# Optimization experiments

Hardware: AMD Instinct MI355X
Metric: run time of the kernel (lower is better)

Reference implementation:

```python
import jax, jax.numpy as jnp
import numpy as np

NBITS = 4
GROUP_SIZE = 128


def setup_inputs() -> dict:
    key = jax.random.key(0)
    k1, k2, k3, k4, k5 = jax.random.split(key, 5)
    B, S, K, N = 2, 2048, 4096, 4096
    G = K // GROUP_SIZE  # 32 groups along K
    x = jax.random.normal(k1, (B, S, K), dtype=jnp.float16)
    # unpacked uint4 weights stored in int32 carrier, values in [0, 2^nbits)
    W_q = jax.random.randint(k2, (N, K), 0, 2 ** NBITS, dtype=jnp.int32)
    scale = (jax.random.uniform(k3, (N, G), dtype=jnp.float32) * 0.01 + 0.001).astype(jnp.float16)
    zero = (jax.random.uniform(k4, (N, G), dtype=jnp.float32) * (2 ** NBITS)).astype(jnp.float16)
    bias = jax.random.normal(k5, (N,), dtype=jnp.float16)
    return {"x": x, "W_q": W_q, "scale": scale, "zero": zero, "bias": bias}


def _dequant(W_q, scale, zero):
    # W_q: [N, K] int, scale/zero: [N, K//group_size] fp16
    # zeros_mode='original': W = (W_q - zero) * scale, per group along K
    N, K = W_q.shape
    G = K // GROUP_SIZE
    Wg = W_q.reshape(N, G, GROUP_SIZE).astype(jnp.float16)
    Wd = (Wg - zero[:, :, None]) * scale[:, :, None]
    return Wd.reshape(N, K)


def reference(x, W_q, scale, zero, bias):
    # out = x @ W_deq^T + bias   (layout 'nt': W is [N, K])
    W = _dequant(W_q, scale, zero)            # [N, K] fp16
    out = jnp.einsum('bsk,nk->bsn', x, W)     # [B, S, N] fp16 accum per module config
    return out + bias
```

## Files before the change

### kernel.cpp

```cpp
#include <hip/hip_runtime.h>
#include <hip/hip_bf16.h>


typedef __bf16 bf16x8 __attribute__((ext_vector_type(8)));
typedef float f32x4 __attribute__((ext_vector_type(4)));

#define BM 128
#define BN 128
#define BK 64

static __device__ __forceinline__ int pack_bf16x2(float a, float b) {
    __hip_bfloat162 p = __float22bfloat162_rn(make_float2(a, b));
    int r;
    __builtin_memcpy(&r, &p, 4);
    return r;
}

__global__ __launch_bounds__(256) void prepass_kernel(
    const float* __restrict__ X,
    const int*   __restrict__ Wq,
    const float* __restrict__ scale,
    const float* __restrict__ zero,
    unsigned short* __restrict__ Ad,
    unsigned short* __restrict__ Wd,
    int K, int G, int GROUP, int nWBlocks)
{
    const int b = blockIdx.x;
    if (b < nWBlocks) {
        const unsigned int idx = (unsigned int)b * 256u + threadIdx.x;
        const unsigned int f = idx * 8u;
        const unsigned int n = f / (unsigned int)K;
        const unsigned int k = f - n * (unsigned int)K;
        const unsigned int g = k / (unsigned int)GROUP;
        const float s  = scale[(size_t)n * G + g];
        const float z  = zero [(size_t)n * G + g];
        const float mz = -z * s;
        const int4 q0 = *(const int4*)(Wq + f);
        const int4 q1 = *(const int4*)(Wq + f + 4);
        int4 d;
        d.x = pack_bf16x2((float)q0.x * s + mz, (float)q0.y * s + mz);
        d.y = pack_bf16x2((float)q0.z * s + mz, (float)q0.w * s + mz);
        d.z = pack_bf16x2((float)q1.x * s + mz, (float)q1.y * s + mz);
        d.w = pack_bf16x2((float)q1.z * s + mz, (float)q1.w * s + mz);
        *(int4*)(Wd + f) = d;
    } else {
        const unsigned int idx = (unsigned int)(b - nWBlocks) * 256u + threadIdx.x;
        const unsigned int f = idx * 8u;
        const float4 a0 = *(const float4*)(X + f);
        const float4 a1 = *(const float4*)(X + f + 4);
        int4 d;
        d.x = pack_bf16x2(a0.x, a0.y);
        d.y = pack_bf16x2(a0.z, a0.w);
        d.z = pack_bf16x2(a1.x, a1.y);
        d.w = pack_bf16x2(a1.z, a1.w);
        *(int4*)(Ad + f) = d;
    }
}

__global__ __launch_bounds__(256, 2) void gemm_bf16_nt(
    const unsigned short* __restrict__ A,
    const unsigned short* __restrict__ Bw,
    const float* __restrict__ bias,
    float*       __restrict__ C,
    int M, int N, int K)
{
    __shared__ unsigned short ldsA[BM * BK];
    __shared__ unsigned short ldsB[BN * BK];

    const int tid   = threadIdx.x;
    const int lane  = tid & 63;
    const int wave  = tid >> 6;
    const int waveM = wave >> 1;
    const int waveN = wave & 1;

    const int blockN0 = blockIdx.x * BN;
    const int blockM0 = blockIdx.y * BM;

    const long long aBase = (long long)blockM0 * K;
    const long long bBase = (long long)blockN0 * K;

    const int rowInChunk = lane >> 3;
    const int col8       = ((lane & 7) ^ rowInChunk) * 8;

    f32x4 acc[4][4];
#pragma unroll
    for (int i = 0; i < 4; ++i)
#pragma unroll
        for (int j = 0; j < 4; ++j)
            acc[i][j] = (f32x4){0.f, 0.f, 0.f, 0.f};

    const int row16 = lane & 15;
    const int quad  = lane >> 4;
    const int sw    = row16 & 7;

    for (int k0 = 0; k0 < K; k0 += BK) {
        __syncthreads();
#pragma unroll
        for (int c = 0; c < 4; ++c) {
            const int chunk = (wave << 2) | c;
            const int row   = (chunk << 3) | rowInChunk;
            const unsigned short* gA = A  + aBase + (long long)row * K + k0 + col8;
            const unsigned short* gB = Bw + bBase + (long long)row * K + k0 + col8;
            __builtin_amdgcn_global_load_lds(
                (const __attribute__((address_space(1))) unsigned int*)gA,
                (__attribute__((address_space(3))) unsigned int*)&ldsA[chunk * 512],
                16, 0, 0);
            __builtin_amdgcn_global_load_lds(
                (const __attribute__((address_space(1))) unsigned int*)gB,
                (__attribute__((address_space(3))) unsigned int*)&ldsB[chunk * 512],
                16, 0, 0);
        }
        __syncthreads();

#pragma unroll
        for (int kk = 0; kk < 2; ++kk) {
            bf16x8 av[4], bv[4];
            const int slot = (kk * 4 + quad) ^ sw;
#pragma unroll
            for (int i = 0; i < 4; ++i) {
                const int r = waveM * 64 + i * 16 + row16;
                av[i] = *(const bf16x8*)&ldsA[r * BK + slot * 8];
            }
#pragma unroll
            for (int j = 0; j < 4; ++j) {
                const int r = waveN * 64 + j * 16 + row16;
                bv[j] = *(const bf16x8*)&ldsB[r * BK + slot * 8];
            }
#pragma unroll
            for (int i = 0; i < 4; ++i)
#pragma unroll
                for (int j = 0; j < 4; ++j)
                    acc[i][j] = __builtin_amdgcn_mfma_f32_16x16x32_bf16(
                        av[i], bv[j], acc[i][j], 0, 0, 0);
        }
    }

    const int colBase = blockN0 + waveN * 64;
    const int rowBase = blockM0 + waveM * 64;
    float biasf[4];
#pragma unroll
    for (int j = 0; j < 4; ++j)
        biasf[j] = bias[colBase + j * 16 + row16];

#pragma unroll
    for (int i = 0; i < 4; ++i) {
        const int row0 = rowBase + i * 16 + quad * 4;
#pragma unroll
        for (int j = 0; j < 4; ++j) {
            const int col = colBase + j * 16 + row16;
#pragma unroll
            for (int r = 0; r < 4; ++r) {
                C[(long long)(row0 + r) * N + col] = acc[i][j][r] + biasf[j];
            }
        }
    }
}

__global__ __launch_bounds__(256) void hqq_gemm_fused_f32(
    const float* __restrict__ A,
    const int*   __restrict__ Wq,
    const float* __restrict__ scale,
    const float* __restrict__ zero,
    const float* __restrict__ bias,
    float*       __restrict__ C,
    int M, int N, int K, int G, int GROUP)
{
    __shared__ unsigned short ldsA[BM * BK];
    __shared__ unsigned short ldsB[BN * BK];

    const int tid   = threadIdx.x;
    const int lane  = tid & 63;
    const int wave  = tid >> 6;
    const int waveM = wave >> 1;
    const int waveN = wave & 1;

    const int blockN0 = blockIdx.x * BN;
    const int blockM0 = blockIdx.y * BM;

    const int row16 = lane & 15;
    const int quad  = lane >> 4;

    f32x4 acc[4][4];
#pragma unroll
    for (int i = 0; i < 4; ++i)
#pragma unroll
        for (int j = 0; j < 4; ++j)
            acc[i][j] = (f32x4){0.f, 0.f, 0.f, 0.f};

    for (int k0 = 0; k0 < K; k0 += BK) {
        const int g = k0 / GROUP;
        int4 ra[4], rb[4];
#pragma unroll
        for (int c = 0; c < 4; ++c) {
            const int chunk = c * 256 + tid;
            const int row   = chunk >> 3;
            const int col   = (chunk & 7) * 8;

            const float* ap = A + (long long)(blockM0 + row) * K + k0 + col;
            const float4 a0 = *(const float4*)(ap);
            const float4 a1 = *(const float4*)(ap + 4);
            int4 da;
            da.x = pack_bf16x2(a0.x, a0.y);
            da.y = pack_bf16x2(a0.z, a0.w);
            da.z = pack_bf16x2(a1.x, a1.y);
            da.w = pack_bf16x2(a1.z, a1.w);
            ra[c] = da;

            const int n = blockN0 + row;
            const float s  = scale[(long long)n * G + g];
            const float z  = zero [(long long)n * G + g];
            const float mz = -z * s;
            const long long wb = (long long)n * K + k0 + col;
            const int4 q0 = *(const int4*)(Wq + wb);
            const int4 q1 = *(const int4*)(Wq + wb + 4);
            int4 db;
            db.x = pack_bf16x2((float)q0.x * s + mz, (float)q0.y * s + mz);
            db.y = pack_bf16x2((float)q0.z * s + mz, (float)q0.w * s + mz);
            db.z = pack_bf16x2((float)q1.x * s + mz, (float)q1.y * s + mz);
            db.w = pack_bf16x2((float)q1.z * s + mz, (float)q1.w * s + mz);
            rb[c] = db;
        }

        __syncthreads();
#pragma unroll
        for (int c = 0; c < 4; ++c) {
            const int chunk = c * 256 + tid;
            *(int4*)&ldsA[chunk * 8] = ra[c];
            *(int4*)&ldsB[chunk * 8] = rb[c];
        }
        __syncthreads();

#pragma unroll
        for (int kk = 0; kk < 2; ++kk) {
            const int kOff = kk * 32 + quad * 8;
            bf16x8 av[4], bv[4];
#pragma unroll
            for (int i = 0; i < 4; ++i)
                av[i] = *(const bf16x8*)&ldsA[(waveM * 64 + i * 16 + row16) * BK + kOff];
#pragma unroll
            for (int j = 0; j < 4; ++j)
                bv[j] = *(const bf16x8*)&ldsB[(waveN * 64 + j * 16 + row16) * BK + kOff];
#pragma unroll
            for (int i = 0; i < 4; ++i)
#pragma unroll
                for (int j = 0; j < 4; ++j)
                    acc[i][j] = __builtin_amdgcn_mfma_f32_16x16x32_bf16(
                        av[i], bv[j], acc[i][j], 0, 0, 0);
        }
    }

    const int colBase = blockN0 + waveN * 64;
    const int rowBase = blockM0 + waveM * 64;
    float biasf[4];
#pragma unroll
    for (int j = 0; j < 4; ++j)
        biasf[j] = bias[colBase + j * 16 + row16];

#pragma unroll
    for (int i = 0; i < 4; ++i) {
        const int row0 = rowBase + i * 16 + quad * 4;
#pragma unroll
        for (int j = 0; j < 4; ++j) {
            const int col = colBase + j * 16 + row16;
#pragma unroll
            for (int r = 0; r < 4; ++r) {
                C[(long long)(row0 + r) * N + col] = acc[i][j][r] + biasf[j];
            }
        }
    }
}

extern "C" void kernel_launch(void* const* d_in, const int* in_sizes, int n_in,
                              void* d_out, int out_size, void* d_ws, size_t ws_size,
                              hipStream_t stream) {
    (void)n_in; (void)out_size;

    const float* x     = (const float*)d_in[0];
    const int*   Wq    = (const int*)d_in[1];
    const float* scale = (const float*)d_in[2];
    const float* zero  = (const float*)d_in[3];
    const float* bias  = (const float*)d_in[4];
    float*       out   = (float*)d_out;

    const int N     = in_sizes[4];
    const int G     = in_sizes[2] / N;
    const int K     = in_sizes[1] / N;
    const int M     = in_sizes[0] / K;
    const int GROUP = K / G;

    const size_t needWs = (size_t)N * K * 2 + (size_t)M * K * 2;

    if (ws_size >= needWs) {
        unsigned short* Wd = (unsigned short*)d_ws;
        unsigned short* Ad = (unsigned short*)((char*)d_ws + (size_t)N * K * 2);

        const int nWBlocks = (int)((long long)N * K / 8 / 256);
        const int nABlocks = (int)((long long)M * K / 8 / 256);
        prepass_kernel<<<nWBlocks + nABlocks, 256, 0, stream>>>(
            x, Wq, scale, zero, Ad, Wd, K, G, GROUP, nWBlocks);

        dim3 grid(N / BN, M / BM);
        gemm_bf16_nt<<<grid, 256, 0, stream>>>(Ad, Wd, bias, out, M, N, K);
    } else {
        dim3 grid(N / BN, M / BM);
        hqq_gemm_fused_f32<<<grid, 256, 0, stream>>>(x, Wq, scale, zero, bias, out,
                                                     M, N, K, G, GROUP);
    }
}
```

Measured before the change: 299.2 us.

## Register-prefetch next GEMM tile and widen prepass to 16 elements per thread

The GEMM main loop now loads the next K-tile from global memory into registers while the current tile is being computed, then writes those registers to LDS. This replaces the direct global_load_lds path and is meant to hide global load latency behind the MFMA work. The prepass kernel also converts 16 elements per thread instead of 8, halving the block count. The trade-offs are higher register pressure, which may hurt occupancy at 2 blocks per SM, and an extra register-to-LDS store step.

```diff
diff --git a/kernel.cpp b/kernel.cpp
--- a/kernel.cpp
+++ b/kernel.cpp
@@ -28,7 +28,7 @@
     const int b = blockIdx.x;
     if (b < nWBlocks) {
         const unsigned int idx = (unsigned int)b * 256u + threadIdx.x;
-        const unsigned int f = idx * 8u;
+        const unsigned int f = idx * 16u;
         const unsigned int n = f / (unsigned int)K;
         const unsigned int k = f - n * (unsigned int)K;
         const unsigned int g = k / (unsigned int)GROUP;
@@ -37,23 +37,37 @@
         const float mz = -z * s;
         const int4 q0 = *(const int4*)(Wq + f);
         const int4 q1 = *(const int4*)(Wq + f + 4);
-        int4 d;
-        d.x = pack_bf16x2((float)q0.x * s + mz, (float)q0.y * s + mz);
-        d.y = pack_bf16x2((float)q0.z * s + mz, (float)q0.w * s + mz);
-        d.z = pack_bf16x2((float)q1.x * s + mz, (float)q1.y * s + mz);
-        d.w = pack_bf16x2((float)q1.z * s + mz, (float)q1.w * s + mz);
-        *(int4*)(Wd + f) = d;
+        const int4 q2 = *(const int4*)(Wq + f + 8);
+        const int4 q3 = *(const int4*)(Wq + f + 12);
+        int4 d0, d1;
+        d0.x = pack_bf16x2((float)q0.x * s + mz, (float)q0.y * s + mz);
+        d0.y = pack_bf16x2((float)q0.z * s + mz, (float)q0.w * s + mz);
+        d0.z = pack_bf16x2((float)q1.x * s + mz, (float)q1.y * s + mz);
+        d0.w = pack_bf16x2((float)q1.z * s + mz, (float)q1.w * s + mz);
+        d1.x = pack_bf16x2((float)q2.x * s + mz, (float)q2.y * s + mz);
+        d1.y = pack_bf16x2((float)q2.z * s + mz, (float)q2.w * s + mz);
+        d1.z = pack_bf16x2((float)q3.x * s + mz, (float)q3.y * s + mz);
+        d1.w = pack_bf16x2((float)q3.z * s + mz, (float)q3.w * s + mz);
+        *(int4*)(Wd + f)     = d0;
+        *(int4*)(Wd + f + 8) = d1;
     } else {
         const unsigned int idx = (unsigned int)(b - nWBlocks) * 256u + threadIdx.x;
-        const unsigned int f = idx * 8u;
+        const unsigned int f = idx * 16u;
         const float4 a0 = *(const float4*)(X + f);
         const float4 a1 = *(const float4*)(X + f + 4);
-        int4 d;
-        d.x = pack_bf16x2(a0.x, a0.y);
-        d.y = pack_bf16x2(a0.z, a0.w);
-        d.z = pack_bf16x2(a1.x, a1.y);
-        d.w = pack_bf16x2(a1.z, a1.w);
-        *(int4*)(Ad + f) = d;
+        const float4 a2 = *(const float4*)(X + f + 8);
+        const float4 a3 = *(const float4*)(X + f + 12);
+        int4 d0, d1;
+        d0.x = pack_bf16x2(a0.x, a0.y);
+        d0.y = pack_bf16x2(a0.z, a0.w);
+        d0.z = pack_bf16x2(a1.x, a1.y);
+        d0.w = pack_bf16x2(a1.z, a1.w);
+        d1.x = pack_bf16x2(a2.x, a2.y);
+        d1.y = pack_bf16x2(a2.z, a2.w);
+        d1.z = pack_bf16x2(a3.x, a3.y);
+        d1.w = pack_bf16x2(a3.z, a3.w);
+        *(int4*)(Ad + f)     = d0;
+        *(int4*)(Ad + f + 8) = d1;
     }
 }
 
@@ -79,8 +93,9 @@
     const long long aBase = (long long)blockM0 * K;
     const long long bBase = (long long)blockN0 * K;
 
-    const int rowInChunk = lane >> 3;
-    const int col8       = ((lane & 7) ^ rowInChunk) * 8;
+    const int trow = tid >> 3;
+    const int tgc  = tid & 7;
+    const int tsw  = tgc ^ (trow & 7);
 
     f32x4 acc[4][4];
 #pragma unroll
@@ -93,24 +108,33 @@
     const int quad  = lane >> 4;
     const int sw    = row16 & 7;
 
+    int4 ra[4], rb[4];
+#pragma unroll
+    for (int c = 0; c < 4; ++c) {
+        const long long r = (long long)(c * 32 + trow) * K + tgc * 8;
+        ra[c] = *(const int4*)(A  + aBase + r);
+        rb[c] = *(const int4*)(Bw + bBase + r);
+    }
+
     for (int k0 = 0; k0 < K; k0 += BK) {
         __syncthreads();
 #pragma unroll
         for (int c = 0; c < 4; ++c) {
-            const int chunk = (wave << 2) | c;
-            const int row   = (chunk << 3) | rowInChunk;
-            const unsigned short* gA = A  + aBase + (long long)row * K + k0 + col8;
-            const unsigned short* gB = Bw + bBase + (long long)row * K + k0 + col8;
-            __builtin_amdgcn_global_load_lds(
-                (const __attribute__((address_space(1))) unsigned int*)gA,
-                (__attribute__((address_space(3))) unsigned int*)&ldsA[chunk * 512],
-                16, 0, 0);
-            __builtin_amdgcn_global_load_lds(
-                (const __attribute__((address_space(1))) unsigned int*)gB,
-                (__attribute__((address_space(3))) unsigned int*)&ldsB[chunk * 512],
-                16, 0, 0);
+            const int ofs = (c * 32 + trow) * BK + tsw * 8;
+            *(int4*)&ldsA[ofs] = ra[c];
+            *(int4*)&ldsB[ofs] = rb[c];
         }
         __syncthreads();
+
+        if (k0 + BK < K) {
+            const long long kn = k0 + BK;
+#pragma unroll
+            for (int c = 0; c < 4; ++c) {
+                const long long r = (long long)(c * 32 + trow) * K + kn + tgc * 8;
+                ra[c] = *(const int4*)(A  + aBase + r);
+                rb[c] = *(const int4*)(Bw + bBase + r);
+            }
+        }
 
 #pragma unroll
         for (int kk = 0; kk < 2; ++kk) {
@@ -294,8 +318,8 @@
         unsigned short* Wd = (unsigned short*)d_ws;
         unsigned short* Ad = (unsigned short*)((char*)d_ws + (size_t)N * K * 2);
 
-        const int nWBlocks = (int)((long long)N * K / 8 / 256);
-        const int nABlocks = (int)((long long)M * K / 8 / 256);
+        const int nWBlocks = (int)((long long)N * K / 16 / 256);
+        const int nABlocks = (int)((long long)M * K / 16 / 256);
         prepass_kernel<<<nWBlocks + nABlocks, 256, 0, stream>>>(
             x, Wq, scale, zero, Ad, Wd, K, G, GROUP, nWBlocks);
 
```

Result: slower. 762.0 us (+154.7%).
